# Kernel tuning notes

Measured on AMD Instinct MI355X. Metric: run time of the kernel, lower is better.

Reference implementation:

```python
import jax, jax.numpy as jnp
import numpy as np

N = 16384
D_IN = 512
HEADS = 2
D_HEAD = 256
EPS_LN = 1e-5
NEG_SLOPE = 0.2


def l2norm_dim0(x):
    # F.normalize(x, p=2, dim=0): per-column L2 normalization
    n = jnp.sqrt(jnp.sum(x * x, axis=0, keepdims=True))
    return x / jnp.maximum(n, 1e-12)


def layer_norm(x, g, b):
    m = jnp.mean(x, axis=-1, keepdims=True)
    v = jnp.mean((x - m) ** 2, axis=-1, keepdims=True)
    return (x - m) * jax.lax.rsqrt(v + EPS_LN) * g + b


def gat_conv(x, edge_index, W, att_src, att_dst, bias):
    # PyG GATConv with add_self_loops=True, concat=True, negative_slope=0.2
    n = x.shape[0]
    loops = jnp.arange(n, dtype=edge_index.dtype)
    src = jnp.concatenate([edge_index[0], loops])
    dst = jnp.concatenate([edge_index[1], loops])
    h = (x @ W).reshape(n, HEADS, D_HEAD)            # [N, H, Dh]
    a_src = jnp.sum(h * att_src, axis=-1)            # [N, H]
    a_dst = jnp.sum(h * att_dst, axis=-1)            # [N, H]
    e = a_src[src] + a_dst[dst]                      # [E, H]
    e = jnp.where(e >= 0, e, NEG_SLOPE * e)          # leaky_relu
    # segment softmax over incoming edges of each dst node
    emax = jax.ops.segment_max(e, dst, num_segments=n)
    ex = jnp.exp(e - emax[dst])
    den = jax.ops.segment_sum(ex, dst, num_segments=n)
    alpha = ex / den[dst]                            # [E, H]
    msg = h[src] * alpha[:, :, None]                 # [E, H, Dh]
    out = jax.ops.segment_sum(msg, dst, num_segments=n)  # [N, H, Dh]
    return out.reshape(n, HEADS * D_HEAD) + bias


def setup_inputs() -> dict:
    key = jax.random.key(0)
    ks = jax.random.split(key, 16)
    def glorot(k, shape):
        lim = np.sqrt(6.0 / (shape[0] + shape[-1]))
        return jax.random.uniform(k, shape, jnp.float32, -lim, lim)
    x = jax.random.normal(ks[0], (N, D_IN), jnp.float32)
    edge_index = jax.random.randint(ks[1], (2, 524288), 0, N, jnp.int64)
    return {
        "x": x,
        "edge_index": edge_index,
        "W": glorot(ks[2], (D_IN, HEADS * D_HEAD)),
        "att_src": glorot(ks[3], (HEADS, D_HEAD)),
        "att_dst": glorot(ks[4], (HEADS, D_HEAD)),
        "bias_conv": jnp.zeros((HEADS * D_HEAD,), jnp.float32),
        "Wa": glorot(ks[5], (512, 256)), "ba": jnp.zeros((256,), jnp.float32),
        "ga": jnp.ones((256,), jnp.float32), "bga": jnp.zeros((256,), jnp.float32),
        "W1": glorot(ks[6], (256, 128)), "b1": jnp.zeros((128,), jnp.float32),
        "g1": jnp.ones((128,), jnp.float32), "bg1": jnp.zeros((128,), jnp.float32),
        "W2": glorot(ks[7], (128, 64)), "b2": jnp.zeros((64,), jnp.float32),
        "g2": jnp.ones((64,), jnp.float32), "bg2": jnp.zeros((64,), jnp.float32),
        "W3": glorot(ks[8], (64, 3)), "b3": jnp.zeros((3,), jnp.float32),
    }


def reference(x, edge_index, W, att_src, att_dst, bias_conv,
              Wa, ba, ga, bga, W1, b1, g1, bg1,
              W2, b2, g2, bg2, W3, b3):
    h = l2norm_dim0(x)
    h = gat_conv(h, edge_index, W, att_src, att_dst, bias_conv)
    h = jax.nn.relu(h)
    h = l2norm_dim0(h)
    h = layer_norm(h @ Wa + ba, ga, bga)
    h = jax.nn.relu(h)
    h = l2norm_dim0(h)
    h = layer_norm(h @ W1 + b1, g1, bg1)
    h = jax.nn.relu(h)
    h = l2norm_dim0(h)
    h = layer_norm(h @ W2 + b2, g2, bg2)
    h = jax.nn.relu(h)
    h = l2norm_dim0(h)
    h = h @ W3 + b3                                  # [N, 3]
    # torch.cdist(h, h, p=2)
    sq = jnp.sum(h * h, axis=-1)
    d2 = sq[:, None] + sq[None, :] - 2.0 * (h @ h.T)
    return jnp.sqrt(jnp.maximum(d2, 0.0))
```

## Files before the change

### kernel.cpp

```cpp
#include <hip/hip_runtime.h>
#include <math.h>


typedef __bf16 bf16x8 __attribute__((ext_vector_type(8)));
typedef __bf16 bf16x4 __attribute__((ext_vector_type(4)));
typedef __bf16 bf16x2 __attribute__((ext_vector_type(2)));
typedef float  f32x4  __attribute__((ext_vector_type(4)));
typedef short  short8 __attribute__((ext_vector_type(8)));

static __device__ __forceinline__ float leaky02(float e){ return e >= 0.f ? e : 0.2f*e; }

static __device__ __forceinline__ float wred_sum(float v){
  #pragma unroll
  for (int m = 1; m < 64; m <<= 1) v += __shfl_xor(v, m);
  return v;
}
static __device__ __forceinline__ float wred_max(float v){
  #pragma unroll
  for (int m = 1; m < 64; m <<= 1) v = fmaxf(v, __shfl_xor(v, m));
  return v;
}

__global__ void colnorm_sq(const float* __restrict__ X, float* __restrict__ ss, int R, int C){
  int c = blockIdx.x*blockDim.x + threadIdx.x;
  if (c >= C) return;
  int r0 = blockIdx.y * 128;
  int r1 = r0 + 128; if (r1 > R) r1 = R;
  float s = 0.f;
  for (int r = r0; r < r1; ++r){ float v = X[(size_t)r*C + c]; s = fmaf(v, v, s); }
  atomicAdd(&ss[c], s);
}

__global__ void colnorm_sq_hl(const __bf16* __restrict__ H, const __bf16* __restrict__ L,
                              float* __restrict__ ss, int R, int C){
  int c = blockIdx.x*blockDim.x + threadIdx.x;
  if (c >= C) return;
  int r0 = blockIdx.y * 128;
  int r1 = r0 + 128; if (r1 > R) r1 = R;
  float s = 0.f;
  for (int r = r0; r < r1; ++r){
    float v = (float)H[(size_t)r*C + c] + (float)L[(size_t)r*C + c];
    s = fmaf(v, v, s);
  }
  atomicAdd(&ss[c], s);
}

__global__ __launch_bounds__(256) void split_tr_scaled(const float* __restrict__ B,
    const float* __restrict__ ss,
    __bf16* __restrict__ TH, __bf16* __restrict__ TL, int K, int N){
  __shared__ float tile[32][33];
  int lx = threadIdx.x & 31, ly = threadIdx.x >> 5;
  int kb = blockIdx.y*32, nb = blockIdx.x*32;
  #pragma unroll
  for (int i = 0; i < 4; i++){
    int kr = kb + ly + i*8;
    float inv = 1.f / fmaxf(sqrtf(ss[kr]), 1e-12f);
    tile[ly + i*8][lx] = B[(size_t)kr*N + nb + lx] * inv;
  }
  __syncthreads();
  #pragma unroll
  for (int i = 0; i < 4; i++){
    int nl = ly + i*8;
    float v = tile[lx][nl];
    __bf16 h = (__bf16)v;
    TH[(size_t)(nb + nl)*K + kb + lx] = h;
    TL[(size_t)(nb + nl)*K + kb + lx] = (__bf16)(v - (float)h);
  }
}

__global__ __launch_bounds__(256) void gemm_bf16x3(
    const __bf16* __restrict__ Ah, const __bf16* __restrict__ Al,
    const __bf16* __restrict__ Bth, const __bf16* __restrict__ Btl,
    float* __restrict__ C, int M, int N, int K)
{
  __shared__ __align__(16) __bf16 sAh[128][40];
  __shared__ __align__(16) __bf16 sAl[128][40];
  __shared__ __align__(16) __bf16 sBh[64][40];
  __shared__ __align__(16) __bf16 sBl[64][40];
  int tid = threadIdx.x;
  int lane = tid & 63, wave = tid >> 6;
  int wr = wave >> 1, wc = wave & 1;
  int rowBase = blockIdx.x << 7, colBase = blockIdx.y << 6;

  int ar = tid >> 2;
  int ac = tid & 3;

  short8 rAh0, rAh1, rAl0, rAl1, rBh, rBl;
  auto loadA = [&](int k0){
    rAh0 = *(const short8*)(Ah + (size_t)(rowBase + ar     )*K + k0 + ac*8);
    rAh1 = *(const short8*)(Ah + (size_t)(rowBase + ar + 64)*K + k0 + ac*8);
    rAl0 = *(const short8*)(Al + (size_t)(rowBase + ar     )*K + k0 + ac*8);
    rAl1 = *(const short8*)(Al + (size_t)(rowBase + ar + 64)*K + k0 + ac*8);
    rBh  = *(const short8*)(Bth + (size_t)(colBase + ar)*K + k0 + ac*8);
    rBl  = *(const short8*)(Btl + (size_t)(colBase + ar)*K + k0 + ac*8);
  };

  f32x4 acc[4][2];
  #pragma unroll
  for (int m = 0; m < 4; m++)
    #pragma unroll
    for (int n = 0; n < 2; n++) acc[m][n] = (f32x4){0.f,0.f,0.f,0.f};

  loadA(0);
  int nsteps = K >> 5;
  for (int s = 0; s < nsteps; ++s){
    __syncthreads();
    *(short8*)&sAh[ar][ac*8]      = rAh0;
    *(short8*)&sAh[ar+64][ac*8]   = rAh1;
    *(short8*)&sAl[ar][ac*8]      = rAl0;
    *(short8*)&sAl[ar+64][ac*8]   = rAl1;
    *(short8*)&sBh[ar][ac*8]      = rBh;
    *(short8*)&sBl[ar][ac*8]      = rBl;
    if (s + 1 < nsteps) loadA((s+1) << 5);
    __syncthreads();

    int kslot = lane >> 4;
    bf16x8 fah[4], fal[4], fbh[2], fbl[2];
    #pragma unroll
    for (int m = 0; m < 4; m++){
      int r = wr*64 + m*16 + (lane & 15);
      fah[m] = *(const bf16x8*)&sAh[r][kslot*8];
      fal[m] = *(const bf16x8*)&sAl[r][kslot*8];
    }
    #pragma unroll
    for (int n = 0; n < 2; n++){
      int c = wc*32 + n*16 + (lane & 15);
      fbh[n] = *(const bf16x8*)&sBh[c][kslot*8];
      fbl[n] = *(const bf16x8*)&sBl[c][kslot*8];
    }
    #pragma unroll
    for (int m = 0; m < 4; m++)
      #pragma unroll
      for (int n = 0; n < 2; n++){
        acc[m][n] = __builtin_amdgcn_mfma_f32_16x16x32_bf16(fah[m], fbh[n], acc[m][n], 0,0,0);
        acc[m][n] = __builtin_amdgcn_mfma_f32_16x16x32_bf16(fah[m], fbl[n], acc[m][n], 0,0,0);
        acc[m][n] = __builtin_amdgcn_mfma_f32_16x16x32_bf16(fal[m], fbh[n], acc[m][n], 0,0,0);
      }
  }

  int rg = lane >> 4, cl = lane & 15;
  #pragma unroll
  for (int m = 0; m < 4; m++)
    #pragma unroll
    for (int n = 0; n < 2; n++)
      #pragma unroll
      for (int j = 0; j < 4; j++)
        C[(size_t)(rowBase + wr*64 + m*16 + rg*4 + j)*N + colBase + wc*32 + n*16 + cl] = acc[m][n][j];
}

__global__ __launch_bounds__(256) void gemm_f32a_bf16x3(
    const float* __restrict__ A,
    const __bf16* __restrict__ Bth, const __bf16* __restrict__ Btl,
    float* __restrict__ C, int M, int N, int K)
{
  __shared__ __align__(16) __bf16 sAh[128][40];
  __shared__ __align__(16) __bf16 sAl[128][40];
  __shared__ __align__(16) __bf16 sBh[64][40];
  __shared__ __align__(16) __bf16 sBl[64][40];
  int tid = threadIdx.x;
  int lane = tid & 63, wave = tid >> 6;
  int wr = wave >> 1, wc = wave & 1;
  int rowBase = blockIdx.x << 7, colBase = blockIdx.y << 6;

  int ar = tid >> 2;
  int ac = tid & 3;

  float4 rA0a, rA0b, rA1a, rA1b; short8 rBh, rBl;
  auto loadA = [&](int k0){
    const float* p0 = A + (size_t)(rowBase + ar)*K + k0 + ac*8;
    rA0a = *(const float4*)p0; rA0b = *(const float4*)(p0 + 4);
    const float* p1 = A + (size_t)(rowBase + ar + 64)*K + k0 + ac*8;
    rA1a = *(const float4*)p1; rA1b = *(const float4*)(p1 + 4);
    rBh  = *(const short8*)(Bth + (size_t)(colBase + ar)*K + k0 + ac*8);
    rBl  = *(const short8*)(Btl + (size_t)(colBase + ar)*K + k0 + ac*8);
  };
  auto splitst = [&](float4 a, float4 b, __bf16* dh, __bf16* dl){
    float t[8] = {a.x,a.y,a.z,a.w,b.x,b.y,b.z,b.w};
    bf16x8 hv, lv;
    #pragma unroll
    for (int j = 0; j < 8; j++){
      __bf16 h = (__bf16)t[j]; hv[j] = h; lv[j] = (__bf16)(t[j] - (float)h);
    }
    *(bf16x8*)dh = hv; *(bf16x8*)dl = lv;
  };

  f32x4 acc[4][2];
  #pragma unroll
  for (int m = 0; m < 4; m++)
    #pragma unroll
    for (int n = 0; n < 2; n++) acc[m][n] = (f32x4){0.f,0.f,0.f,0.f};

  loadA(0);
  int nsteps = K >> 5;
  for (int s = 0; s < nsteps; ++s){
    __syncthreads();
    splitst(rA0a, rA0b, &sAh[ar][ac*8],    &sAl[ar][ac*8]);
    splitst(rA1a, rA1b, &sAh[ar+64][ac*8], &sAl[ar+64][ac*8]);
    *(short8*)&sBh[ar][ac*8] = rBh;
    *(short8*)&sBl[ar][ac*8] = rBl;
    if (s + 1 < nsteps) loadA((s+1) << 5);
    __syncthreads();

    int kslot = lane >> 4;
    bf16x8 fah[4], fal[4], fbh[2], fbl[2];
    #pragma unroll
    for (int m = 0; m < 4; m++){
      int r = wr*64 + m*16 + (lane & 15);
      fah[m] = *(const bf16x8*)&sAh[r][kslot*8];
      fal[m] = *(const bf16x8*)&sAl[r][kslot*8];
    }
    #pragma unroll
    for (int n = 0; n < 2; n++){
      int c = wc*32 + n*16 + (lane & 15);
      fbh[n] = *(const bf16x8*)&sBh[c][kslot*8];
      fbl[n] = *(const bf16x8*)&sBl[c][kslot*8];
    }
    #pragma unroll
    for (int m = 0; m < 4; m++)
      #pragma unroll
      for (int n = 0; n < 2; n++){
        acc[m][n] = __builtin_amdgcn_mfma_f32_16x16x32_bf16(fah[m], fbh[n], acc[m][n], 0,0,0);
        acc[m][n] = __builtin_amdgcn_mfma_f32_16x16x32_bf16(fah[m], fbl[n], acc[m][n], 0,0,0);
        acc[m][n] = __builtin_amdgcn_mfma_f32_16x16x32_bf16(fal[m], fbh[n], acc[m][n], 0,0,0);
      }
  }

  int rg = lane >> 4, cl = lane & 15;
  #pragma unroll
  for (int m = 0; m < 4; m++)
    #pragma unroll
    for (int n = 0; n < 2; n++)
      #pragma unroll
      for (int j = 0; j < 4; j++)
        C[(size_t)(rowBase + wr*64 + m*16 + rg*4 + j)*N + colBase + wc*32 + n*16 + cl] = acc[m][n][j];
}

__global__ __launch_bounds__(256) void att_kernel(const float* __restrict__ h,
    const float* __restrict__ att_src, const float* __restrict__ att_dst,
    float* __restrict__ asrc, float* __restrict__ adst, int N){
  int lane = threadIdx.x & 63;
  int node = blockIdx.x*4 + (threadIdx.x >> 6);
  const float4* hp = (const float4*)(h + (size_t)node*512);
  float4 v0 = hp[lane], v1 = hp[64 + lane];
  float4 as0 = ((const float4*)att_src)[lane], as1 = ((const float4*)att_src)[64+lane];
  float4 ad0 = ((const float4*)att_dst)[lane], ad1 = ((const float4*)att_dst)[64+lane];
  float s0 = v0.x*as0.x + v0.y*as0.y + v0.z*as0.z + v0.w*as0.w;
  float s1 = v1.x*as1.x + v1.y*as1.y + v1.z*as1.z + v1.w*as1.w;
  float d0 = v0.x*ad0.x + v0.y*ad0.y + v0.z*ad0.z + v0.w*ad0.w;
  float d1 = v1.x*ad1.x + v1.y*ad1.y + v1.z*ad1.z + v1.w*ad1.w;
  s0 = wred_sum(s0); s1 = wred_sum(s1); d0 = wred_sum(d0); d1 = wred_sum(d1);
  if (lane == 0){
    asrc[2*node] = s0; asrc[2*node+1] = s1;
    adst[2*node] = d0; adst[2*node+1] = d1;
  }
}

__global__ void deg_count(const int* __restrict__ dst, int* deg, int E){
  int e = blockIdx.x*blockDim.x + threadIdx.x;
  if (e < E) atomicAdd(&deg[dst[e]], 1);
}
__global__ __launch_bounds__(1024) void scan_kernel(const int* __restrict__ deg,
    int* __restrict__ offs, int* __restrict__ cursor, int n){
  __shared__ int part[1024];
  int t = threadIdx.x;
  int chunk = (n + 1023) >> 10;
  int base = t * chunk;
  int loc[32];
  int local = 0;
  for (int k = 0; k < chunk; k++){
    int idx = base + k; loc[k] = local;
    if (idx < n) local += deg[idx] + 1;
  }
  part[t] = local; __syncthreads();
  for (int off = 1; off < 1024; off <<= 1){
    int v = (t >= off) ? part[t-off] : 0; __syncthreads();
    part[t] += v; __syncthreads();
  }
  int excl = part[t] - local;
  for (int k = 0; k < chunk; k++){
    int idx = base + k;
    if (idx < n){ int o = excl + loc[k]; offs[idx] = o; cursor[idx] = o; }
  }
  if (t == 1023) offs[n] = part[1023];
}
__global__ void scatter_edges(const int* __restrict__ src, const int* __restrict__ dst,
                              int* cursor, int* __restrict__ ssrc, int E, int N){
  int e = blockIdx.x*blockDim.x + threadIdx.x;
  if (e < E){
    int d = dst[e]; int pos = atomicAdd(&cursor[d], 1); ssrc[pos] = src[e];
  } else if (e < E + N){
    int i = e - E; int pos = atomicAdd(&cursor[i], 1); ssrc[pos] = i;
  }
}

__global__ __launch_bounds__(256) void gat_aggregate_w(const float* __restrict__ h,
    const int* __restrict__ offs, const int* __restrict__ ssrc,
    const float* __restrict__ asrc, const float* __restrict__ adst,
    const float* __restrict__ bias,
    __bf16* __restrict__ H, __bf16* __restrict__ L, int N){
  int lane = threadIdx.x & 63;
  int d = blockIdx.x*4 + (threadIdx.x >> 6);
  int beg = offs[d], end = offs[d+1], cnt = end - beg;
  float ad0 = adst[2*d], ad1 = adst[2*d+1];

  int dbase = lane*8;
  bool head0 = dbase < 256;
  f32x4 acc0 = {0.f,0.f,0.f,0.f}, acc1 = {0.f,0.f,0.f,0.f};

  if (cnt <= 64){
    int sreg = 0; float le0 = -1e30f, le1 = -1e30f;
    if (lane < cnt){
      sreg = ssrc[beg + lane];
      float2 a = *(const float2*)&asrc[2*sreg];
      le0 = leaky02(a.x + ad0); le1 = leaky02(a.y + ad1);
    }
    float m0 = wred_max(le0), m1 = wred_max(le1);
    float e0 = (lane < cnt) ? __expf(le0 - m0) : 0.f;
    float e1 = (lane < cnt) ? __expf(le1 - m1) : 0.f;
    float inv0 = 1.f / wred_sum(e0), inv1 = 1.f / wred_sum(e1);
    float al0 = e0*inv0, al1 = e1*inv1;
    for (int o = 0; o < cnt; ++o){
      int s = __shfl(sreg, o);
      float aA = __shfl(al0, o), aB = __shfl(al1, o);
      float al = head0 ? aA : aB;
      const float4* hp = (const float4*)&h[(size_t)s*512 + dbase];
      float4 v0 = hp[0], v1 = hp[1];
      acc0[0] = fmaf(al, v0.x, acc0[0]); acc0[1] = fmaf(al, v0.y, acc0[1]);
      acc0[2] = fmaf(al, v0.z, acc0[2]); acc0[3] = fmaf(al, v0.w, acc0[3]);
      acc1[0] = fmaf(al, v1.x, acc1[0]); acc1[1] = fmaf(al, v1.y, acc1[1]);
      acc1[2] = fmaf(al, v1.z, acc1[2]); acc1[3] = fmaf(al, v1.w, acc1[3]);
    }
  } else {
    float m0 = -1e30f, m1 = -1e30f;
    for (int o = beg + lane; o < end; o += 64){
      int s = ssrc[o]; float2 a = *(const float2*)&asrc[2*s];
      m0 = fmaxf(m0, leaky02(a.x + ad0)); m1 = fmaxf(m1, leaky02(a.y + ad1));
    }
    m0 = wred_max(m0); m1 = wred_max(m1);
    float q0 = 0.f, q1 = 0.f;
    for (int o = beg + lane; o < end; o += 64){
      int s = ssrc[o]; float2 a = *(const float2*)&asrc[2*s];
      q0 += __expf(leaky02(a.x + ad0) - m0); q1 += __expf(leaky02(a.y + ad1) - m1);
    }
    float inv0 = 1.f / wred_sum(q0), inv1 = 1.f / wred_sum(q1);
    for (int c0 = beg; c0 < end; c0 += 64){
      int cc = end - c0; if (cc > 64) cc = 64;
      int sreg = 0; float al0 = 0.f, al1 = 0.f;
      if (lane < cc){
        sreg = ssrc[c0 + lane];
        float2 a = *(const float2*)&asrc[2*sreg];
        al0 = __expf(leaky02(a.x + ad0) - m0) * inv0;
        al1 = __expf(leaky02(a.y + ad1) - m1) * inv1;
      }
      for (int o = 0; o < cc; ++o){
        int s = __shfl(sreg, o);
        float aA = __shfl(al0, o), aB = __shfl(al1, o);
        float al = head0 ? aA : aB;
        const float4* hp = (const float4*)&h[(size_t)s*512 + dbase];
        float4 v0 = hp[0], v1 = hp[1];
        acc0[0] = fmaf(al, v0.x, acc0[0]); acc0[1] = fmaf(al, v0.y, acc0[1]);
        acc0[2] = fmaf(al, v0.z, acc0[2]); acc0[3] = fmaf(al, v0.w, acc0[3]);
        acc1[0] = fmaf(al, v1.x, acc1[0]); acc1[1] = fmaf(al, v1.y, acc1[1]);
        acc1[2] = fmaf(al, v1.z, acc1[2]); acc1[3] = fmaf(al, v1.w, acc1[3]);
      }
    }
  }

  float4 bi0 = *(const float4*)&bias[dbase];
  float4 bi1 = *(const float4*)&bias[dbase + 4];
  float o_[8];
  o_[0] = fmaxf(acc0[0] + bi0.x, 0.f); o_[1] = fmaxf(acc0[1] + bi0.y, 0.f);
  o_[2] = fmaxf(acc0[2] + bi0.z, 0.f); o_[3] = fmaxf(acc0[3] + bi0.w, 0.f);
  o_[4] = fmaxf(acc1[0] + bi1.x, 0.f); o_[5] = fmaxf(acc1[1] + bi1.y, 0.f);
  o_[6] = fmaxf(acc1[2] + bi1.z, 0.f); o_[7] = fmaxf(acc1[3] + bi1.w, 0.f);
  bf16x8 hv, lv;
  #pragma unroll
  for (int j = 0; j < 8; j++){
    __bf16 hh = (__bf16)o_[j]; hv[j] = hh; lv[j] = (__bf16)(o_[j] - (float)hh);
  }
  *(bf16x8*)&H[(size_t)d*512 + dbase] = hv;
  *(bf16x8*)&L[(size_t)d*512 + dbase] = lv;
}

template<int C, bool SPLIT>
__global__ __launch_bounds__(256) void ln_relu_t(float* __restrict__ Z,
    const float* __restrict__ bias, const float* __restrict__ g,
    const float* __restrict__ bg, __bf16* __restrict__ H, __bf16* __restrict__ L, int R){
  constexpr int VW = C / 64;
  int lane = threadIdx.x & 63, wid = threadIdx.x >> 6;
  int r = blockIdx.x*4 + wid;
  size_t base = (size_t)r*C + lane*VW;
  float v[VW], bi[VW], gm[VW], bt[VW];
  if constexpr (VW == 4){
    float4 t0 = *(const float4*)&Z[base];
    float4 t1 = *(const float4*)&bias[lane*4];
    float4 t2 = *(const float4*)&g[lane*4];
    float4 t3 = *(const float4*)&bg[lane*4];
    v[0]=t0.x; v[1]=t0.y; v[2]=t0.z; v[3]=t0.w;
    bi[0]=t1.x; bi[1]=t1.y; bi[2]=t1.z; bi[3]=t1.w;
    gm[0]=t2.x; gm[1]=t2.y; gm[2]=t2.z; gm[3]=t2.w;
    bt[0]=t3.x; bt[1]=t3.y; bt[2]=t3.z; bt[3]=t3.w;
  } else if constexpr (VW == 2){
    float2 t0 = *(const float2*)&Z[base];
    float2 t1 = *(const float2*)&bias[lane*2];
    float2 t2 = *(const float2*)&g[lane*2];
    float2 t3 = *(const float2*)&bg[lane*2];
    v[0]=t0.x; v[1]=t0.y; bi[0]=t1.x; bi[1]=t1.y;
    gm[0]=t2.x; gm[1]=t2.y; bt[0]=t3.x; bt[1]=t3.y;
  } else {
    v[0] = Z[base]; bi[0] = bias[lane]; gm[0] = g[lane]; bt[0] = bg[lane];
  }
  float sum = 0.f;
  #pragma unroll
  for (int j = 0; j < VW; j++){ v[j] += bi[j]; sum += v[j]; }
  sum = wred_sum(sum);
  float mean = sum * (1.f/C);
  float sq = 0.f;
  #pragma unroll
  for (int j = 0; j < VW; j++){ float dz = v[j]-mean; sq += dz*dz; }
  sq = wred_sum(sq);
  float rs = 1.f / sqrtf(sq*(1.f/C) + 1e-5f);
  float o[VW];
  #pragma unroll
  for (int j = 0; j < VW; j++) o[j] = fmaxf((v[j]-mean)*rs*gm[j] + bt[j], 0.f);
  if constexpr (VW == 4) *(float4*)&Z[base] = make_float4(o[0],o[1],o[2],o[3]);
  else if constexpr (VW == 2) *(float2*)&Z[base] = make_float2(o[0],o[1]);
  else Z[base] = o[0];
  if constexpr (SPLIT){
    if constexpr (VW == 4){
      bf16x4 hv, lv;
      #pragma unroll
      for (int j = 0; j < 4; j++){ hv[j] = (__bf16)o[j]; lv[j] = (__bf16)(o[j]-(float)hv[j]); }
      *(bf16x4*)&H[base] = hv; *(bf16x4*)&L[base] = lv;
    } else if constexpr (VW == 2){
      bf16x2 hv, lv;
      #pragma unroll
      for (int j = 0; j < 2; j++){ hv[j] = (__bf16)o[j]; lv[j] = (__bf16)(o[j]-(float)hv[j]); }
      *(bf16x2*)&H[base] = hv; *(bf16x2*)&L[base] = lv;
    } else {
      __bf16 hv = (__bf16)o[0];
      H[base] = hv; L[base] = (__bf16)(o[0]-(float)hv);
    }
  }
}

__global__ __launch_bounds__(256) void final_hf4(const float* __restrict__ A,
    const float* __restrict__ W3, const float* __restrict__ ss,
    const float* __restrict__ b3, float4* __restrict__ hf4, int N){
  __shared__ float w[64*3];
  __shared__ float b[3];
  if (threadIdx.x < 192){
    int k = threadIdx.x / 3;
    w[threadIdx.x] = W3[threadIdx.x] / fmaxf(sqrtf(ss[k]), 1e-12f);
  }
  if (threadIdx.x < 3) b[threadIdx.x] = b3[threadIdx.x];
  __syncthreads();
  int r = blockIdx.x*blockDim.x + threadIdx.x;
  if (r >= N) return;
  float x = b[0], y = b[1], z = b[2];
  #pragma unroll 8
  for (int k = 0; k < 64; ++k){
    float a = A[(size_t)r*64 + k];
    x = fmaf(a, w[k*3],   x);
    y = fmaf(a, w[k*3+1], y);
    z = fmaf(a, w[k*3+2], z);
  }
  float sq = x*x + y*y + z*z;
  hf4[r] = make_float4(x, y, z, sq);
}

__global__ __launch_bounds__(256) void cdist_kernel(const float4* __restrict__ hf,
                                                    float* __restrict__ out, int N){
  int i = blockIdx.y;
  int j0 = (blockIdx.x*256 + threadIdx.x)*4;
  float4 a = hf[i];
  float4 b0 = hf[j0], b1 = hf[j0+1], b2 = hf[j0+2], b3 = hf[j0+3];
  f32x4 r; float d;
  d = a.w + b0.w - 2.f*(a.x*b0.x + a.y*b0.y + a.z*b0.z); r[0] = sqrtf(fmaxf(d, 0.f));
  d = a.w + b1.w - 2.f*(a.x*b1.x + a.y*b1.y + a.z*b1.z); r[1] = sqrtf(fmaxf(d, 0.f));
  d = a.w + b2.w - 2.f*(a.x*b2.x + a.y*b2.y + a.z*b2.z); r[2] = sqrtf(fmaxf(d, 0.f));
  d = a.w + b3.w - 2.f*(a.x*b3.x + a.y*b3.y + a.z*b3.z); r[3] = sqrtf(fmaxf(d, 0.f));
  __builtin_nontemporal_store(r, (f32x4*)&out[(size_t)i*N + j0]);
}

extern "C" void kernel_launch(void* const* d_in, const int* in_sizes, int n_in,
                              void* d_out, int out_size, void* d_ws, size_t ws_size,
                              hipStream_t stream){
  const int N = in_sizes[0] / 512;
  const int E = in_sizes[1] / 2;

  const float* x         = (const float*)d_in[0];
  const int*   ei        = (const int*)  d_in[1];
  const float* W         = (const float*)d_in[2];
  const float* att_src   = (const float*)d_in[3];
  const float* att_dst   = (const float*)d_in[4];
  const float* bias_conv = (const float*)d_in[5];
  const float* Wa  = (const float*)d_in[6];
  const float* ba  = (const float*)d_in[7];
  const float* ga  = (const float*)d_in[8];
  const float* bga = (const float*)d_in[9];
  const float* W1  = (const float*)d_in[10];
  const float* b1  = (const float*)d_in[11];
  const float* g1  = (const float*)d_in[12];
  const float* bg1 = (const float*)d_in[13];
  const float* W2  = (const float*)d_in[14];
  const float* b2  = (const float*)d_in[15];
  const float* g2  = (const float*)d_in[16];
  const float* bg2 = (const float*)d_in[17];
  const float* W3  = (const float*)d_in[18];
  const float* b3  = (const float*)d_in[19];

  const int* e_src = ei;
  const int* e_dst = ei + E;

  size_t off = 0;
  auto alloc = [&](size_t bytes)->char*{
    size_t o = off; off += (bytes + 255) & ~(size_t)255;
    return (char*)d_ws + o;
  };
  float* bufA  = (float*)alloc((size_t)N*512*4);
  float* bufB  = (float*)alloc((size_t)N*512*4);
  __bf16* Ah   = (__bf16*)alloc((size_t)N*512*2);
  __bf16* Al   = (__bf16*)alloc((size_t)N*512*2);
  __bf16* Bth  = (__bf16*)alloc(512*512*2);
  __bf16* Btl  = (__bf16*)alloc(512*512*2);
  char* zbase  = alloc(5*512*4 + (size_t)N*4);
  float* ss1 = (float*)zbase;
  float* ss2 = ss1 + 512;
  float* ss3 = ss2 + 512;
  float* ss4 = ss3 + 512;
  float* ss5 = ss4 + 512;
  int*   deg = (int*)(ss5 + 512);
  float* asrc  = (float*)alloc((size_t)N*2*4);
  float* adst  = (float*)alloc((size_t)N*2*4);
  float4* hf4  = (float4*)alloc((size_t)N*16);
  int* offs    = (int*)alloc((size_t)(N+1)*4);
  int* cursor  = (int*)alloc((size_t)N*4);
  int* ssrc    = (int*)alloc((size_t)(E+N)*4);

  float* outF = (float*)d_out;

  hipMemsetAsync(zbase, 0, 5*512*4 + (size_t)N*4, stream);

  colnorm_sq<<<dim3(2,128), 256, 0, stream>>>(x, ss1, N, 512);
  split_tr_scaled<<<dim3(16,16), 256, 0, stream>>>(W, ss1, Bth, Btl, 512, 512);
  gemm_f32a_bf16x3<<<dim3(N/128, 8), 256, 0, stream>>>(x, Bth, Btl, bufA, N, 512, 512);

  att_kernel<<<N/4, 256, 0, stream>>>(bufA, att_src, att_dst, asrc, adst, N);
  deg_count<<<(E+255)/256, 256, 0, stream>>>(e_dst, deg, E);
  scan_kernel<<<1, 1024, 0, stream>>>(deg, offs, cursor, N);
  scatter_edges<<<(E+N+255)/256, 256, 0, stream>>>(e_src, e_dst, cursor, ssrc, E, N);
  gat_aggregate_w<<<N/4, 256, 0, stream>>>(bufA, offs, ssrc, asrc, adst, bias_conv,
                                           Ah, Al, N);

  colnorm_sq_hl<<<dim3(2,128), 256, 0, stream>>>(Ah, Al, ss2, N, 512);
  split_tr_scaled<<<dim3(8,16), 256, 0, stream>>>(Wa, ss2, Bth, Btl, 512, 256);
  gemm_bf16x3<<<dim3(N/128, 4), 256, 0, stream>>>(Ah, Al, Bth, Btl, bufB, N, 256, 512);
  ln_relu_t<256,true><<<N/4, 256, 0, stream>>>(bufB, ba, ga, bga, Ah, Al, N);

  colnorm_sq<<<dim3(1,128), 256, 0, stream>>>(bufB, ss3, N, 256);
  split_tr_scaled<<<dim3(4,8), 256, 0, stream>>>(W1, ss3, Bth, Btl, 256, 128);
  gemm_bf16x3<<<dim3(N/128, 2), 256, 0, stream>>>(Ah, Al, Bth, Btl, bufA, N, 128, 256);
  ln_relu_t<128,true><<<N/4, 256, 0, stream>>>(bufA, b1, g1, bg1, Ah, Al, N);

  colnorm_sq<<<dim3(1,128), 256, 0, stream>>>(bufA, ss4, N, 128);
  split_tr_scaled<<<dim3(2,4), 256, 0, stream>>>(W2, ss4, Bth, Btl, 128, 64);
  gemm_bf16x3<<<dim3(N/128, 1), 256, 0, stream>>>(Ah, Al, Bth, Btl, bufB, N, 64, 128);
  ln_relu_t<64,false><<<N/4, 256, 0, stream>>>(bufB, b2, g2, bg2, (__bf16*)nullptr, (__bf16*)nullptr, N);

  colnorm_sq<<<dim3(1,128), 256, 0, stream>>>(bufB, ss5, N, 64);
  final_hf4<<<(N+255)/256, 256, 0, stream>>>(bufB, W3, ss5, b3, hf4, N);
  cdist_kernel<<<dim3(N/1024, N), 256, 0, stream>>>(hf4, outF, N);
}
```

Measured before the change: 761.7 us.

## Fuse column-norm reductions into producer epilogues and merge att/degree kernels

Column sum-of-squares for each L2 normalization is now accumulated in the epilogues of gat_aggregate and ln_relu through shared-memory block reduction and global atomics, which removes four separate colnorm passes that re-read the activations. The attention-score and degree-count kernels are merged into a single launch. The gather loop is also unrolled by four so more row loads are in flight at once. The costs are many more global atomics per column (one per block instead of one per 128 rows) and extra shared memory in the producer kernels.

```diff
diff --git a/kernel.cpp b/kernel.cpp
--- a/kernel.cpp
+++ b/kernel.cpp
@@ -28,20 +28,6 @@
   int r1 = r0 + 128; if (r1 > R) r1 = R;
   float s = 0.f;
   for (int r = r0; r < r1; ++r){ float v = X[(size_t)r*C + c]; s = fmaf(v, v, s); }
-  atomicAdd(&ss[c], s);
-}
-
-__global__ void colnorm_sq_hl(const __bf16* __restrict__ H, const __bf16* __restrict__ L,
-                              float* __restrict__ ss, int R, int C){
-  int c = blockIdx.x*blockDim.x + threadIdx.x;
-  if (c >= C) return;
-  int r0 = blockIdx.y * 128;
-  int r1 = r0 + 128; if (r1 > R) r1 = R;
-  float s = 0.f;
-  for (int r = r0; r < r1; ++r){
-    float v = (float)H[(size_t)r*C + c] + (float)L[(size_t)r*C + c];
-    s = fmaf(v, v, s);
-  }
   atomicAdd(&ss[c], s);
 }
 
@@ -235,30 +221,32 @@
         C[(size_t)(rowBase + wr*64 + m*16 + rg*4 + j)*N + colBase + wc*32 + n*16 + cl] = acc[m][n][j];
 }
 
-__global__ __launch_bounds__(256) void att_kernel(const float* __restrict__ h,
+__global__ __launch_bounds__(256) void att_deg_kernel(const float* __restrict__ h,
     const float* __restrict__ att_src, const float* __restrict__ att_dst,
-    float* __restrict__ asrc, float* __restrict__ adst, int N){
-  int lane = threadIdx.x & 63;
-  int node = blockIdx.x*4 + (threadIdx.x >> 6);
-  const float4* hp = (const float4*)(h + (size_t)node*512);
-  float4 v0 = hp[lane], v1 = hp[64 + lane];
-  float4 as0 = ((const float4*)att_src)[lane], as1 = ((const float4*)att_src)[64+lane];
-  float4 ad0 = ((const float4*)att_dst)[lane], ad1 = ((const float4*)att_dst)[64+lane];
-  float s0 = v0.x*as0.x + v0.y*as0.y + v0.z*as0.z + v0.w*as0.w;
-  float s1 = v1.x*as1.x + v1.y*as1.y + v1.z*as1.z + v1.w*as1.w;
-  float d0 = v0.x*ad0.x + v0.y*ad0.y + v0.z*ad0.z + v0.w*ad0.w;
-  float d1 = v1.x*ad1.x + v1.y*ad1.y + v1.z*ad1.z + v1.w*ad1.w;
-  s0 = wred_sum(s0); s1 = wred_sum(s1); d0 = wred_sum(d0); d1 = wred_sum(d1);
-  if (lane == 0){
-    asrc[2*node] = s0; asrc[2*node+1] = s1;
-    adst[2*node] = d0; adst[2*node+1] = d1;
-  }
-}
-
-__global__ void deg_count(const int* __restrict__ dst, int* deg, int E){
-  int e = blockIdx.x*blockDim.x + threadIdx.x;
-  if (e < E) atomicAdd(&deg[dst[e]], 1);
-}
+    float* __restrict__ asrc, float* __restrict__ adst,
+    const int* __restrict__ dst, int* __restrict__ deg, int nAttBlk, int E){
+  if ((int)blockIdx.x < nAttBlk){
+    int lane = threadIdx.x & 63;
+    int node = blockIdx.x*4 + (threadIdx.x >> 6);
+    const float4* hp = (const float4*)(h + (size_t)node*512);
+    float4 v0 = hp[lane], v1 = hp[64 + lane];
+    float4 as0 = ((const float4*)att_src)[lane], as1 = ((const float4*)att_src)[64+lane];
+    float4 ad0 = ((const float4*)att_dst)[lane], ad1 = ((const float4*)att_dst)[64+lane];
+    float s0 = v0.x*as0.x + v0.y*as0.y + v0.z*as0.z + v0.w*as0.w;
+    float s1 = v1.x*as1.x + v1.y*as1.y + v1.z*as1.z + v1.w*as1.w;
+    float d0 = v0.x*ad0.x + v0.y*ad0.y + v0.z*ad0.z + v0.w*ad0.w;
+    float d1 = v1.x*ad1.x + v1.y*ad1.y + v1.z*ad1.z + v1.w*ad1.w;
+    s0 = wred_sum(s0); s1 = wred_sum(s1); d0 = wred_sum(d0); d1 = wred_sum(d1);
+    if (lane == 0){
+      asrc[2*node] = s0; asrc[2*node+1] = s1;
+      adst[2*node] = d0; adst[2*node+1] = d1;
+    }
+  } else {
+    int e = (blockIdx.x - nAttBlk)*256 + threadIdx.x;
+    if (e < E) atomicAdd(&deg[dst[e]], 1);
+  }
+}
+
 __global__ __launch_bounds__(1024) void scan_kernel(const int* __restrict__ deg,
     int* __restrict__ offs, int* __restrict__ cursor, int n){
   __shared__ int part[1024];
@@ -297,15 +285,68 @@
     const int* __restrict__ offs, const int* __restrict__ ssrc,
     const float* __restrict__ asrc, const float* __restrict__ adst,
     const float* __restrict__ bias,
-    __bf16* __restrict__ H, __bf16* __restrict__ L, int N){
-  int lane = threadIdx.x & 63;
-  int d = blockIdx.x*4 + (threadIdx.x >> 6);
+    __bf16* __restrict__ H, __bf16* __restrict__ L,
+    float* __restrict__ ssOut, int N){
+  __shared__ float sq[4][512];
+  int lane = threadIdx.x & 63, wid = threadIdx.x >> 6;
+  int d = blockIdx.x*4 + wid;
   int beg = offs[d], end = offs[d+1], cnt = end - beg;
   float ad0 = adst[2*d], ad1 = adst[2*d+1];
 
   int dbase = lane*8;
   bool head0 = dbase < 256;
   f32x4 acc0 = {0.f,0.f,0.f,0.f}, acc1 = {0.f,0.f,0.f,0.f};
+
+  auto gather = [&](int sreg, float al0, float al1, int cc){
+    int o = 0;
+    for (; o + 4 <= cc; o += 4){
+      int s_0 = __shfl(sreg, o+0), s_1 = __shfl(sreg, o+1);
+      int s_2 = __shfl(sreg, o+2), s_3 = __shfl(sreg, o+3);
+      float a00 = __shfl(al0, o+0), a10 = __shfl(al1, o+0);
+      float a01 = __shfl(al0, o+1), a11 = __shfl(al1, o+1);
+      float a02 = __shfl(al0, o+2), a12 = __shfl(al1, o+2);
+      float a03 = __shfl(al0, o+3), a13 = __shfl(al1, o+3);
+      float w0 = head0 ? a00 : a10;
+      float w1 = head0 ? a01 : a11;
+      float w2 = head0 ? a02 : a12;
+      float w3 = head0 ? a03 : a13;
+      const float4* p0 = (const float4*)&h[(size_t)s_0*512 + dbase];
+      const float4* p1 = (const float4*)&h[(size_t)s_1*512 + dbase];
+      const float4* p2 = (const float4*)&h[(size_t)s_2*512 + dbase];
+      const float4* p3 = (const float4*)&h[(size_t)s_3*512 + dbase];
+      float4 u00 = p0[0], u01 = p0[1];
+      float4 u10 = p1[0], u11 = p1[1];
+      float4 u20 = p2[0], u21 = p2[1];
+      float4 u30 = p3[0], u31 = p3[1];
+      acc0[0] = fmaf(w0,u00.x,acc0[0]); acc0[1] = fmaf(w0,u00.y,acc0[1]);
+      acc0[2] = fmaf(w0,u00.z,acc0[2]); acc0[3] = fmaf(w0,u00.w,acc0[3]);
+      acc1[0] = fmaf(w0,u01.x,acc1[0]); acc1[1] = fmaf(w0,u01.y,acc1[1]);
+      acc1[2] = fmaf(w0,u01.z,acc1[2]); acc1[3] = fmaf(w0,u01.w,acc1[3]);
+      acc0[0] = fmaf(w1,u10.x,acc0[0]); acc0[1] = fmaf(w1,u10.y,acc0[1]);
+      acc0[2] = fmaf(w1,u10.z,acc0[2]); acc0[3] = fmaf(w1,u10.w,acc0[3]);
+      acc1[0] = fmaf(w1,u11.x,acc1[0]); acc1[1] = fmaf(w1,u11.y,acc1[1]);
+      acc1[2] = fmaf(w1,u11.z,acc1[2]); acc1[3] = fmaf(w1,u11.w,acc1[3]);
+      acc0[0] = fmaf(w2,u20.x,acc0[0]); acc0[1] = fmaf(w2,u20.y,acc0[1]);
+      acc0[2] = fmaf(w2,u20.z,acc0[2]); acc0[3] = fmaf(w2,u20.w,acc0[3]);
+      acc1[0] = fmaf(w2,u21.x,acc1[0]); acc1[1] = fmaf(w2,u21.y,acc1[1]);
+      acc1[2] = fmaf(w2,u21.z,acc1[2]); acc1[3] = fmaf(w2,u21.w,acc1[3]);
+      acc0[0] = fmaf(w3,u30.x,acc0[0]); acc0[1] = fmaf(w3,u30.y,acc0[1]);
+      acc0[2] = fmaf(w3,u30.z,acc0[2]); acc0[3] = fmaf(w3,u30.w,acc0[3]);
+      acc1[0] = fmaf(w3,u31.x,acc1[0]); acc1[1] = fmaf(w3,u31.y,acc1[1]);
+      acc1[2] = fmaf(w3,u31.z,acc1[2]); acc1[3] = fmaf(w3,u31.w,acc1[3]);
+    }
+    for (; o < cc; ++o){
+      int s = __shfl(sreg, o);
+      float aA = __shfl(al0, o), aB = __shfl(al1, o);
+      float w = head0 ? aA : aB;
+      const float4* hp = (const float4*)&h[(size_t)s*512 + dbase];
+      float4 v0 = hp[0], v1 = hp[1];
+      acc0[0] = fmaf(w,v0.x,acc0[0]); acc0[1] = fmaf(w,v0.y,acc0[1]);
+      acc0[2] = fmaf(w,v0.z,acc0[2]); acc0[3] = fmaf(w,v0.w,acc0[3]);
+      acc1[0] = fmaf(w,v1.x,acc1[0]); acc1[1] = fmaf(w,v1.y,acc1[1]);
+      acc1[2] = fmaf(w,v1.z,acc1[2]); acc1[3] = fmaf(w,v1.w,acc1[3]);
+    }
+  };
 
   if (cnt <= 64){
     int sreg = 0; float le0 = -1e30f, le1 = -1e30f;
@@ -318,18 +359,7 @@
     float e0 = (lane < cnt) ? __expf(le0 - m0) : 0.f;
     float e1 = (lane < cnt) ? __expf(le1 - m1) : 0.f;
     float inv0 = 1.f / wred_sum(e0), inv1 = 1.f / wred_sum(e1);
-    float al0 = e0*inv0, al1 = e1*inv1;
-    for (int o = 0; o < cnt; ++o){
-      int s = __shfl(sreg, o);
-      float aA = __shfl(al0, o), aB = __shfl(al1, o);
-      float al = head0 ? aA : aB;
-      const float4* hp = (const float4*)&h[(size_t)s*512 + dbase];
-      float4 v0 = hp[0], v1 = hp[1];
-      acc0[0] = fmaf(al, v0.x, acc0[0]); acc0[1] = fmaf(al, v0.y, acc0[1]);
-      acc0[2] = fmaf(al, v0.z, acc0[2]); acc0[3] = fmaf(al, v0.w, acc0[3]);
-      acc1[0] = fmaf(al, v1.x, acc1[0]); acc1[1] = fmaf(al, v1.y, acc1[1]);
-      acc1[2] = fmaf(al, v1.z, acc1[2]); acc1[3] = fmaf(al, v1.w, acc1[3]);
-    }
+    gather(sreg, e0*inv0, e1*inv1, cnt);
   } else {
     float m0 = -1e30f, m1 = -1e30f;
     for (int o = beg + lane; o < end; o += 64){
@@ -352,17 +382,7 @@
         al0 = __expf(leaky02(a.x + ad0) - m0) * inv0;
         al1 = __expf(leaky02(a.y + ad1) - m1) * inv1;
       }
-      for (int o = 0; o < cc; ++o){
-        int s = __shfl(sreg, o);
-        float aA = __shfl(al0, o), aB = __shfl(al1, o);
-        float al = head0 ? aA : aB;
-        const float4* hp = (const float4*)&h[(size_t)s*512 + dbase];
-        float4 v0 = hp[0], v1 = hp[1];
-        acc0[0] = fmaf(al, v0.x, acc0[0]); acc0[1] = fmaf(al, v0.y, acc0[1]);
-        acc0[2] = fmaf(al, v0.z, acc0[2]); acc0[3] = fmaf(al, v0.w, acc0[3]);
-        acc1[0] = fmaf(al, v1.x, acc1[0]); acc1[1] = fmaf(al, v1.y, acc1[1]);
-        acc1[2] = fmaf(al, v1.z, acc1[2]); acc1[3] = fmaf(al, v1.w, acc1[3]);
-      }
+      gather(sreg, al0, al1, cc);
     }
   }
 
@@ -377,16 +397,25 @@
   #pragma unroll
   for (int j = 0; j < 8; j++){
     __bf16 hh = (__bf16)o_[j]; hv[j] = hh; lv[j] = (__bf16)(o_[j] - (float)hh);
+    sq[wid][dbase + j] = o_[j]*o_[j];
   }
   *(bf16x8*)&H[(size_t)d*512 + dbase] = hv;
   *(bf16x8*)&L[(size_t)d*512 + dbase] = lv;
+  __syncthreads();
+  int t = threadIdx.x;
+  float s0 = sq[0][t] + sq[1][t] + sq[2][t] + sq[3][t];
+  float s1 = sq[0][t+256] + sq[1][t+256] + sq[2][t+256] + sq[3][t+256];
+  atomicAdd(&ssOut[t], s0);
+  atomicAdd(&ssOut[t+256], s1);
 }
 
 template<int C, bool SPLIT>
 __global__ __launch_bounds__(256) void ln_relu_t(float* __restrict__ Z,
     const float* __restrict__ bias, const float* __restrict__ g,
-    const float* __restrict__ bg, __bf16* __restrict__ H, __bf16* __restrict__ L, int R){
+    const float* __restrict__ bg, __bf16* __restrict__ H, __bf16* __restrict__ L,
+    float* __restrict__ ssOut, int R){
   constexpr int VW = C / 64;
+  __shared__ float sls[4][C];
   int lane = threadIdx.x & 63, wid = threadIdx.x >> 6;
   int r = blockIdx.x*4 + wid;
   size_t base = (size_t)r*C + lane*VW;
@@ -441,6 +470,14 @@
       __bf16 hv = (__bf16)o[0];
       H[base] = hv; L[base] = (__bf16)(o[0]-(float)hv);
     }
+  }
+  #pragma unroll
+  for (int j = 0; j < VW; j++) sls[wid][lane*VW + j] = o[j]*o[j];
+  __syncthreads();
+  int t = threadIdx.x;
+  if (t < C){
+    float s = sls[0][t] + sls[1][t] + sls[2][t] + sls[3][t];
+    atomicAdd(&ssOut[t], s);
   }
 }
 
@@ -546,29 +583,27 @@
   split_tr_scaled<<<dim3(16,16), 256, 0, stream>>>(W, ss1, Bth, Btl, 512, 512);
   gemm_f32a_bf16x3<<<dim3(N/128, 8), 256, 0, stream>>>(x, Bth, Btl, bufA, N, 512, 512);
 
-  att_kernel<<<N/4, 256, 0, stream>>>(bufA, att_src, att_dst, asrc, adst, N);
-  deg_count<<<(E+255)/256, 256, 0, stream>>>(e_dst, deg, E);
+  int nAttBlk = N/4;
+  att_deg_kernel<<<nAttBlk + (E+255)/256, 256, 0, stream>>>(bufA, att_src, att_dst,
+                                                            asrc, adst, e_dst, deg, nAttBlk, E);
   scan_kernel<<<1, 1024, 0, stream>>>(deg, offs, cursor, N);
   scatter_edges<<<(E+N+255)/256, 256, 0, stream>>>(e_src, e_dst, cursor, ssrc, E, N);
   gat_aggregate_w<<<N/4, 256, 0, stream>>>(bufA, offs, ssrc, asrc, adst, bias_conv,
-                                           Ah, Al, N);
-
-  colnorm_sq_hl<<<dim3(2,128), 256, 0, stream>>>(Ah, Al, ss2, N, 512);
+                                           Ah, Al, ss2, N);
+
   split_tr_scaled<<<dim3(8,16), 256, 0, stream>>>(Wa, ss2, Bth, Btl, 512, 256);
   gemm_bf16x3<<<dim3(N/128, 4), 256, 0, stream>>>(Ah, Al, Bth, Btl, bufB, N, 256, 512);
-  ln_relu_t<256,true><<<N/4, 256, 0, stream>>>(bufB, ba, ga, bga, Ah, Al, N);
-
-  colnorm_sq<<<dim3(1,128), 256, 0, stream>>>(bufB, ss3, N, 256);
+  ln_relu_t<256,true><<<N/4, 256, 0, stream>>>(bufB, ba, ga, bga, Ah, Al, ss3, N);
+
   split_tr_scaled<<<dim3(4,8), 256, 0, stream>>>(W1, ss3, Bth, Btl, 256, 128);
   gemm_bf16x3<<<dim3(N/128, 2), 256, 0, stream>>>(Ah, Al, Bth, Btl, bufA, N, 128, 256);
-  ln_relu_t<128,true><<<N/4, 256, 0, stream>>>(bufA, b1, g1, bg1, Ah, Al, N);
-
-  colnorm_sq<<<dim3(1,128), 256, 0, stream>>>(bufA, ss4, N, 128);
+  ln_relu_t<128,true><<<N/4, 256, 0, stream>>>(bufA, b1, g1, bg1, Ah, Al, ss4, N);
+
   split_tr_scaled<<<dim3(2,4), 256, 0, stream>>>(W2, ss4, Bth, Btl, 128, 64);
   gemm_bf16x3<<<dim3(N/128, 1), 256, 0, stream>>>(Ah, Al, Bth, Btl, bufB, N, 64, 128);
-  ln_relu_t<64,false><<<N/4, 256, 0, stream>>>(bufB, b2, g2, bg2, (__bf16*)nullptr, (__bf16*)nullptr, N);
-
-  colnorm_sq<<<dim3(1,128), 256, 0, stream>>>(bufB, ss5, N, 64);
+  ln_relu_t<64,false><<<N/4, 256, 0, stream>>>(bufB, b2, g2, bg2,
+                                               (__bf16*)nullptr, (__bf16*)nullptr, ss5, N);
+
   final_hf4<<<(N+255)/256, 256, 0, stream>>>(bufB, W3, ss5, b3, hf4, N);
   cdist_kernel<<<dim3(N/1024, N), 256, 0, stream>>>(hf4, outF, N);
 }
```

Measured after the change: 927.9 us. 21.8% more time.
